# Performance work log

Hardware: AMD Instinct MI355X
Metric: run time of the kernel (lower is better)

The kernel has to match this reference:

```python
import jax, jax.numpy as jnp
import numpy as np

HEAD_SIZE = 64

def setup_inputs() -> dict:
    key = jax.random.key(0)
    k1, k2, k3, k4 = jax.random.split(key, 4)
    B, S, D = 8, 2048, 1024
    scale = 1.0 / np.sqrt(D)
    x = jax.random.normal(k1, (B, S, D), dtype=jnp.float32)
    Wk = jax.random.normal(k2, (D, HEAD_SIZE), dtype=jnp.float32) * scale
    Wq = jax.random.normal(k3, (D, HEAD_SIZE), dtype=jnp.float32) * scale
    Wv = jax.random.normal(k4, (D, HEAD_SIZE), dtype=jnp.float32) * scale
    return {"x": x, "Wk": Wk, "Wq": Wq, "Wv": Wv}

def reference(x, Wk, Wq, Wv):
    # x: [B, S, D]; projections to [B, S, H]
    k = jnp.einsum('bsd,dh->bsh', x, Wk)
    q = jnp.einsum('bsd,dh->bsh', x, Wq)
    v = jnp.einsum('bsd,dh->bsh', x, Wv)
    H = q.shape[-1]
    scores = jnp.einsum('bqh,bkh->bqk', q, k) / jnp.sqrt(jnp.float32(H))  # [B,S,S]
    S = scores.shape[-1]
    causal = jnp.tril(jnp.ones((S, S), dtype=bool))
    scores = jnp.where(causal, scores, -jnp.inf)
    attn = jax.nn.softmax(scores, axis=-1)
    z = jnp.einsum('bqk,bkh->bqh', attn, v)  # [B,S,H]
    return z
```

## Files before the change

kernel.cpp:

```cpp
#include <hip/hip_runtime.h>
#include <hip/hip_bf16.h>

#define B_ 8
#define S_ 2048
#define D_ 1024
#define H_ 64

typedef __attribute__((ext_vector_type(8))) short bf16x8;
typedef __attribute__((ext_vector_type(4))) float f32x4;
typedef __attribute__((ext_vector_type(4))) unsigned short u16x4;
typedef unsigned short u16;
typedef unsigned int u32;

#define QSCALE 0.18033688011112042f

static __device__ __forceinline__ u16 f2bf(float f) {
  union { float f; unsigned u; } v; v.f = f;
  unsigned r = v.u + 0x7FFFu + ((v.u >> 16) & 1u);
  return (u16)(r >> 16);
}

__global__ __launch_bounds__(256) void wprep_kernel(const float* __restrict__ Wk,
                                                    const float* __restrict__ Wq,
                                                    const float* __restrict__ Wv,
                                                    u16* __restrict__ Wt) {
  const int c = blockIdx.x;
  const float* W = (c < 64) ? Wq : ((c < 128) ? Wk : Wv);
  const int cc = c & 63;
  for (int d = threadIdx.x; d < D_; d += blockDim.x)
    Wt[c * D_ + d] = f2bf(W[d * H_ + cc]);
}

__global__ __launch_bounds__(512, 4) void qkv_kernel(const float* __restrict__ x,
                                                     const u16* __restrict__ Wt,
                                                     u16* __restrict__ Qb,
                                                     u16* __restrict__ Kb,
                                                     u16* __restrict__ Vt) {
  __shared__ char sh[65536];
  char* const xsb = sh;
  char* const wsb = sh + 16384;

  const int tid = threadIdx.x;
  const int w = tid >> 6;
  const int lane = tid & 63;
  const int r = lane & 15;
  const int g = lane >> 4;
  const int rg = w >> 2;
  const int cg = w & 3;

  const int bpin = blockIdx.x & 7;
  const int jj = blockIdx.x >> 3;
  const long row0 = ((long)bpin * 64 + jj) * 32;

#define STAGE_X(kc, buf)                                                       \
  {                                                                            \
    const char* gb = (const char*)x + (size_t)row0 * 4096 + (size_t)(kc) * 256;\
    const int L = tid * 16;                                                    \
    const int row = L >> 8;                                                    \
    const int sw = (L & 255) ^ ((row & 7) << 4);                               \
    __builtin_amdgcn_global_load_lds(                                          \
        (const __attribute__((address_space(1))) u32*)(gb + (size_t)row * 4096 + sw), \
        (__attribute__((address_space(3))) u32*)(xsb + (buf) * 8192 + L),      \
        16, 0, 0);                                                             \
  }

#define STAGE_W(kc, buf)                                                       \
  {                                                                            \
    const char* gb = (const char*)Wt + (size_t)(kc) * 128;                     \
    _Pragma("unroll") for (int j2 = 0; j2 < 3; ++j2) {                         \
      const int L = j2 * 8192 + tid * 16;                                      \
      const int col = L >> 7;                                                  \
      const int sw = (L & 127) ^ ((col & 7) << 4);                             \
      __builtin_amdgcn_global_load_lds(                                        \
          (const __attribute__((address_space(1))) u32*)(gb + (size_t)col * 2048 + sw), \
          (__attribute__((address_space(3))) u32*)(wsb + (buf) * 24576 + L),   \
          16, 0, 0);                                                           \
    }                                                                          \
  }

  f32x4 acc[3];
#pragma unroll
  for (int nf = 0; nf < 3; ++nf) acc[nf] = (f32x4){0.f, 0.f, 0.f, 0.f};

  STAGE_X(0, 0);
  STAGE_W(0, 0);
  int cur = 0;

  const int rr = rg * 16 + r;
  const int xswz = (rr & 7) << 4;

  for (int kc = 0; kc < 16; ++kc) {
    __syncthreads();
    if (kc < 15) {
      STAGE_X(kc + 1, cur ^ 1);
      STAGE_W(kc + 1, cur ^ 1);
    }
    __builtin_amdgcn_sched_barrier(0);

    const char* xb = xsb + cur * 8192;
    const char* wb = wsb + cur * 24576;
#pragma unroll
    for (int ks = 0; ks < 2; ++ks) {
      const int cb = ks * 128 + g * 32;
      const float4 lo = *(const float4*)(xb + rr * 256 + (cb ^ xswz));
      const float4 hi = *(const float4*)(xb + rr * 256 + ((cb + 16) ^ xswz));
      bf16x8 a;
      a[0] = (short)f2bf(lo.x); a[1] = (short)f2bf(lo.y);
      a[2] = (short)f2bf(lo.z); a[3] = (short)f2bf(lo.w);
      a[4] = (short)f2bf(hi.x); a[5] = (short)f2bf(hi.y);
      a[6] = (short)f2bf(hi.z); a[7] = (short)f2bf(hi.w);
#pragma unroll
      for (int nf = 0; nf < 3; ++nf) {
        const int col = cg * 48 + nf * 16 + r;
        const int wcb = (ks * 64 + g * 16) ^ ((col & 7) << 4);
        const bf16x8 b = *(const bf16x8*)(wb + col * 128 + wcb);
        acc[nf] = __builtin_amdgcn_mfma_f32_16x16x32_bf16(a, b, acc[nf], 0, 0, 0);
      }
    }
    cur ^= 1;
  }
#undef STAGE_W
#undef STAGE_X

  const int bb = (int)(row0 >> 11);
  const int srow = (int)(row0 & 2047) + rg * 16;
#pragma unroll
  for (int nf = 0; nf < 3; ++nf) {
    const int col = cg * 48 + nf * 16 + r;
    if (col < 64) {
#pragma unroll
      for (int ii = 0; ii < 4; ++ii)
        Qb[(row0 + rg * 16 + 4 * g + ii) * H_ + col] = f2bf(acc[nf][ii] * QSCALE);
    } else if (col < 128) {
#pragma unroll
      for (int ii = 0; ii < 4; ++ii)
        Kb[(row0 + rg * 16 + 4 * g + ii) * H_ + (col - 64)] = f2bf(acc[nf][ii]);
    } else {
      u16x4 vp;
#pragma unroll
      for (int ii = 0; ii < 4; ++ii) vp[ii] = f2bf(acc[nf][ii]);
      *(u16x4*)(Vt + ((size_t)(bb * H_ + (col - 128))) * S_ + srow + 4 * g) = vp;
    }
  }
}

__global__ __launch_bounds__(256, 2) void attn7_kernel(const u16* __restrict__ Qb,
                                                       const u16* __restrict__ Kb,
                                                       const u16* __restrict__ Vt,
                                                       float* __restrict__ out) {
  __shared__ u16 plds[4][16 * 72];
  __shared__ float plo[4][16][68];
  __shared__ float pml[4][2][16];

  const int b = blockIdx.x & 7;
  const int j = blockIdx.x >> 3;
  const int w = threadIdx.x >> 6;
  const int lane = threadIdx.x & 63;
  const int r = lane & 15;
  const int g = lane >> 4;

  const int qt = (w < 2) ? j : (127 - j);
  const int s = w & 1;
  const int q0 = qt << 4;
  const int T = (qt >> 2) + 1;
  const int half = (T + 1) >> 1;
  const int start = s ? half : 0;
  const int end = s ? T : half;

  const u16* Qp = Qb + ((long)(b * S_ + q0 + r)) * H_ + 8 * g;
  const bf16x8 bq0 = *(const bf16x8*)Qp;
  const bf16x8 bq1 = *(const bf16x8*)(Qp + 32);

  const u16* Kbase = Kb + (long)b * S_ * H_ + (long)r * H_ + 8 * g;
  const u16* Vbase = Vt + (long)b * H_ * S_ + (long)r * S_ + 8 * g;

  f32x4 o[4];
#pragma unroll
  for (int nf = 0; nf < 4; ++nf) o[nf] = (f32x4){0.f, 0.f, 0.f, 0.f};
  float m = -INFINITY, l = 0.f;

  u16* pw = plds[w];

  bf16x8 ka[8];
  if (start < end) {
    const int k0 = start << 6;
#pragma unroll
    for (int kf = 0; kf < 4; ++kf) {
      const u16* Kp = Kbase + (long)(k0 + kf * 16) * H_;
      ka[2 * kf] = *(const bf16x8*)(Kp);
      ka[2 * kf + 1] = *(const bf16x8*)(Kp + 32);
    }
  }

  for (int kt = start; kt < end; ++kt) {
    const int k0 = kt << 6;

    f32x4 t4[4];
#pragma unroll
    for (int kf = 0; kf < 4; ++kf) {
      f32x4 t = (f32x4){0.f, 0.f, 0.f, 0.f};
      t = __builtin_amdgcn_mfma_f32_16x16x32_bf16(ka[2 * kf], bq0, t, 0, 0, 0);
      t = __builtin_amdgcn_mfma_f32_16x16x32_bf16(ka[2 * kf + 1], bq1, t, 0, 0, 0);
      t4[kf] = t;
    }

    bf16x8 vv[8];
#pragma unroll
    for (int nf = 0; nf < 4; ++nf) {
      const u16* Vp = Vbase + (long)(nf * 16) * S_ + k0;
      vv[2 * nf] = *(const bf16x8*)(Vp);
      vv[2 * nf + 1] = *(const bf16x8*)(Vp + 32);
    }
    if (kt + 1 < end) {
      const int kn = (kt + 1) << 6;
#pragma unroll
      for (int kf = 0; kf < 4; ++kf) {
        const u16* Kp = Kbase + (long)(kn + kf * 16) * H_;
        ka[2 * kf] = *(const bf16x8*)(Kp);
        ka[2 * kf + 1] = *(const bf16x8*)(Kp + 32);
      }
    }

    if (kt == T - 1) {
#pragma unroll
      for (int kf = 0; kf < 4; ++kf)
#pragma unroll
        for (int i = 0; i < 4; ++i) {
          const int k = k0 + kf * 16 + 4 * g + i;
          if (k > q0 + r) t4[kf][i] = -INFINITY;
        }
    }

    float pm = t4[0][0];
#pragma unroll
    for (int kf = 0; kf < 4; ++kf)
#pragma unroll
      for (int i = 0; i < 4; ++i) pm = fmaxf(pm, t4[kf][i]);
    pm = fmaxf(pm, __shfl_xor(pm, 16));
    pm = fmaxf(pm, __shfl_xor(pm, 32));

    if (__any(pm > m + 8.f)) {
      const float mn = fmaxf(m, pm);
      const float sc = exp2f(m - mn);
      m = mn;
      l *= sc;
      float scr[4];
#pragma unroll
      for (int i = 0; i < 4; ++i) scr[i] = __shfl(sc, 4 * g + i);
#pragma unroll
      for (int nf = 0; nf < 4; ++nf)
#pragma unroll
        for (int i = 0; i < 4; ++i) o[nf][i] *= scr[i];
    }

    float ps = 0.f;
#pragma unroll
    for (int kf = 0; kf < 4; ++kf)
#pragma unroll
      for (int i = 0; i < 4; ++i) {
        const float p = exp2f(t4[kf][i] - m);
        t4[kf][i] = p;
        ps += p;
      }
    ps += __shfl_xor(ps, 16);
    ps += __shfl_xor(ps, 32);
    l += ps;

#pragma unroll
    for (int kf = 0; kf < 4; ++kf) {
      u16x4 pk;
#pragma unroll
      for (int i = 0; i < 4; ++i) pk[i] = f2bf(t4[kf][i]);
      *(u16x4*)(pw + r * 72 + kf * 16 + 4 * g) = pk;
    }

    const bf16x8 pa0 = *(const bf16x8*)(pw + r * 72 + 8 * g);
    const bf16x8 pa1 = *(const bf16x8*)(pw + r * 72 + 32 + 8 * g);

#pragma unroll
    for (int nf = 0; nf < 4; ++nf) {
      o[nf] = __builtin_amdgcn_mfma_f32_16x16x32_bf16(pa0, vv[2 * nf], o[nf], 0, 0, 0);
      o[nf] = __builtin_amdgcn_mfma_f32_16x16x32_bf16(pa1, vv[2 * nf + 1], o[nf], 0, 0, 0);
    }
  }

#pragma unroll
  for (int nf = 0; nf < 4; ++nf)
#pragma unroll
    for (int i = 0; i < 4; ++i)
      plo[w][4 * g + i][nf * 16 + r] = o[nf][i];
  if (g == 0) {
    pml[w][0][r] = m;
    pml[w][1][r] = l;
  }
  __syncthreads();

  const int base = (w >> 1) << 1;
  const int hlf = w & 1;
  const int qq0 = ((base == 0) ? j : (127 - j)) << 4;
#pragma unroll
  for (int rr = 0; rr < 8; ++rr) {
    const int row = hlf * 8 + rr;
    const float mA = pml[base][0][row], mB = pml[base + 1][0][row];
    const float lA = pml[base][1][row], lB = pml[base + 1][1][row];
    const float M = fmaxf(mA, mB);
    const float ea = exp2f(mA - M), eb = exp2f(mB - M);
    const float inv = 1.f / (lA * ea + lB * eb);
    const float oo = plo[base][row][lane] * ea + plo[base + 1][row][lane] * eb;
    out[((long)(b * S_ + qq0 + row)) * H_ + lane] = oo * inv;
  }
}

extern "C" void kernel_launch(void* const* d_in, const int* in_sizes, int n_in,
                              void* d_out, int out_size, void* d_ws, size_t ws_size,
                              hipStream_t stream) {
  const float* x  = (const float*)d_in[0];
  const float* Wk = (const float*)d_in[1];
  const float* Wq = (const float*)d_in[2];
  const float* Wv = (const float*)d_in[3];
  float* out = (float*)d_out;

  u16* Qb = (u16*)d_ws;
  u16* Kb = Qb + (long)B_ * S_ * H_;
  u16* Vt = Kb + (long)B_ * S_ * H_;
  u16* Wt = Vt + (long)B_ * S_ * H_;

  wprep_kernel<<<192, 256, 0, stream>>>(Wk, Wq, Wv, Wt);
  qkv_kernel<<<512, 512, 0, stream>>>(x, Wt, Qb, Kb, Vt);
  attn7_kernel<<<B_ * 64, 256, 0, stream>>>(Qb, Kb, Vt, out);
}
```

Baseline: 60.94 us.

## Triple-buffer QKV projection staging with explicit vmcnt waits; prioritize attention MFMAs

The QKV projection kernel moves from double to triple buffering of the x and W tiles in LDS, prefetching two k-chunks ahead. It uses raw s_barrier with explicit s_waitcnt vmcnt counts so that loads still in flight are not drained at every step. LDS per block grows to about 96 KB and the occupancy hint drops from 4 to 2 blocks. The attention kernel also wraps its MFMA bursts in s_setprio so matrix work gets issue priority over other waves.

After: 75.26 us. 23.5% more time.

```diff
diff --git a/kernel.cpp b/kernel.cpp
--- a/kernel.cpp
+++ b/kernel.cpp
@@ -31,14 +31,13 @@
     Wt[c * D_ + d] = f2bf(W[d * H_ + cc]);
 }
 
-__global__ __launch_bounds__(512, 4) void qkv_kernel(const float* __restrict__ x,
+__global__ __launch_bounds__(512, 2) void qkv_kernel(const float* __restrict__ x,
                                                      const u16* __restrict__ Wt,
                                                      u16* __restrict__ Qb,
                                                      u16* __restrict__ Kb,
                                                      u16* __restrict__ Vt) {
-  __shared__ char sh[65536];
-  char* const xsb = sh;
-  char* const wsb = sh + 16384;
+  __shared__ __attribute__((aligned(16))) char xs3[3][8192];
+  __shared__ __attribute__((aligned(16))) char ws3[3][24576];
 
   const int tid = threadIdx.x;
   const int w = tid >> 6;
@@ -52,53 +51,55 @@
   const int jj = blockIdx.x >> 3;
   const long row0 = ((long)bpin * 64 + jj) * 32;
 
-#define STAGE_X(kc, buf)                                                       \
+#define STAGE_ALL(kc)                                                          \
   {                                                                            \
-    const char* gb = (const char*)x + (size_t)row0 * 4096 + (size_t)(kc) * 256;\
-    const int L = tid * 16;                                                    \
-    const int row = L >> 8;                                                    \
-    const int sw = (L & 255) ^ ((row & 7) << 4);                               \
-    __builtin_amdgcn_global_load_lds(                                          \
-        (const __attribute__((address_space(1))) u32*)(gb + (size_t)row * 4096 + sw), \
-        (__attribute__((address_space(3))) u32*)(xsb + (buf) * 8192 + L),      \
-        16, 0, 0);                                                             \
-  }
-
-#define STAGE_W(kc, buf)                                                       \
-  {                                                                            \
-    const char* gb = (const char*)Wt + (size_t)(kc) * 128;                     \
-    _Pragma("unroll") for (int j2 = 0; j2 < 3; ++j2) {                         \
-      const int L = j2 * 8192 + tid * 16;                                      \
-      const int col = L >> 7;                                                  \
-      const int sw = (L & 127) ^ ((col & 7) << 4);                             \
+    const int bsel = (kc) % 3;                                                 \
+    {                                                                          \
+      const char* gb = (const char*)x + (size_t)row0 * 4096 + (size_t)(kc) * 256; \
+      const int L = tid * 16;                                                  \
+      const int row = L >> 8;                                                  \
+      const int sw = (L & 255) ^ ((row & 7) << 4);                             \
       __builtin_amdgcn_global_load_lds(                                        \
-          (const __attribute__((address_space(1))) u32*)(gb + (size_t)col * 2048 + sw), \
-          (__attribute__((address_space(3))) u32*)(wsb + (buf) * 24576 + L),   \
+          (const __attribute__((address_space(1))) u32*)(gb + (size_t)row * 4096 + sw), \
+          (__attribute__((address_space(3))) u32*)(&xs3[bsel][0] + L),         \
           16, 0, 0);                                                           \
     }                                                                          \
+    {                                                                          \
+      const char* gb = (const char*)Wt + (size_t)(kc) * 128;                   \
+      _Pragma("unroll") for (int j2 = 0; j2 < 3; ++j2) {                       \
+        const int L = j2 * 8192 + tid * 16;                                    \
+        const int col = L >> 7;                                                \
+        const int sw = (L & 127) ^ ((col & 7) << 4);                           \
+        __builtin_amdgcn_global_load_lds(                                      \
+            (const __attribute__((address_space(1))) u32*)(gb + (size_t)col * 2048 + sw), \
+            (__attribute__((address_space(3))) u32*)(&ws3[bsel][0] + L),       \
+            16, 0, 0);                                                         \
+      }                                                                        \
+    }                                                                          \
   }
 
   f32x4 acc[3];
 #pragma unroll
   for (int nf = 0; nf < 3; ++nf) acc[nf] = (f32x4){0.f, 0.f, 0.f, 0.f};
 
-  STAGE_X(0, 0);
-  STAGE_W(0, 0);
-  int cur = 0;
+  STAGE_ALL(0);
+  STAGE_ALL(1);
 
   const int rr = rg * 16 + r;
   const int xswz = (rr & 7) << 4;
 
   for (int kc = 0; kc < 16; ++kc) {
-    __syncthreads();
-    if (kc < 15) {
-      STAGE_X(kc + 1, cur ^ 1);
-      STAGE_W(kc + 1, cur ^ 1);
-    }
+    __builtin_amdgcn_s_barrier();
     __builtin_amdgcn_sched_barrier(0);
-
-    const char* xb = xsb + cur * 8192;
-    const char* wb = wsb + cur * 24576;
+    if (kc + 2 < 16) STAGE_ALL(kc + 2);
+    if (kc <= 13) asm volatile("s_waitcnt vmcnt(8)" ::: "memory");
+    else if (kc == 14) asm volatile("s_waitcnt vmcnt(4)" ::: "memory");
+    else asm volatile("s_waitcnt vmcnt(0)" ::: "memory");
+    __builtin_amdgcn_s_barrier();
+    __builtin_amdgcn_sched_barrier(0);
+
+    const char* xb = &xs3[kc % 3][0];
+    const char* wb = &ws3[kc % 3][0];
 #pragma unroll
     for (int ks = 0; ks < 2; ++ks) {
       const int cb = ks * 128 + g * 32;
@@ -117,10 +118,8 @@
         acc[nf] = __builtin_amdgcn_mfma_f32_16x16x32_bf16(a, b, acc[nf], 0, 0, 0);
       }
     }
-    cur ^= 1;
-  }
-#undef STAGE_W
-#undef STAGE_X
+  }
+#undef STAGE_ALL
 
   const int bb = (int)(row0 >> 11);
   const int srow = (int)(row0 & 2047) + rg * 16;
@@ -196,6 +195,7 @@
     const int k0 = kt << 6;
 
     f32x4 t4[4];
+    __builtin_amdgcn_s_setprio(1);
 #pragma unroll
     for (int kf = 0; kf < 4; ++kf) {
       f32x4 t = (f32x4){0.f, 0.f, 0.f, 0.f};
@@ -203,6 +203,7 @@
       t = __builtin_amdgcn_mfma_f32_16x16x32_bf16(ka[2 * kf + 1], bq1, t, 0, 0, 0);
       t4[kf] = t;
     }
+    __builtin_amdgcn_s_setprio(0);
 
     bf16x8 vv[8];
 #pragma unroll
@@ -277,11 +278,13 @@
     const bf16x8 pa0 = *(const bf16x8*)(pw + r * 72 + 8 * g);
     const bf16x8 pa1 = *(const bf16x8*)(pw + r * 72 + 32 + 8 * g);
 
+    __builtin_amdgcn_s_setprio(1);
 #pragma unroll
     for (int nf = 0; nf < 4; ++nf) {
       o[nf] = __builtin_amdgcn_mfma_f32_16x16x32_bf16(pa0, vv[2 * nf], o[nf], 0, 0, 0);
       o[nf] = __builtin_amdgcn_mfma_f32_16x16x32_bf16(pa1, vv[2 * nf + 1], o[nf], 0, 0, 0);
     }
+    __builtin_amdgcn_s_setprio(0);
   }
 
 #pragma unroll
```
